# Kernel optimization log

Measured on AMD Instinct MI355X. Metric: run time of the kernel, lower is better.

Reference implementation:

```python
import jax, jax.numpy as jnp
import numpy as np

DN = ('NCHW', 'OIHW', 'NCHW')  # conv dimension numbers
EPS = 1e-5


def _tcn(x, w1, b1, w2, b2, w3, b3):
    """Gated TCN. x: [B,T,N,C] -> [B,T-2,N,Cout].  out = conv1(x)*sigmoid(conv2(x)) + tanh(conv3(x))"""
    xc = jnp.transpose(x, (0, 3, 2, 1))  # [B,C,N,T]
    conv = lambda w, b: jax.lax.conv_general_dilated(xc, w, (1, 1), 'VALID', dimension_numbers=DN) + b[None, :, None, None]
    p = conv(w1, b1)
    q = jax.nn.sigmoid(conv(w2, b2))
    r = jnp.tanh(conv(w3, b3))
    out = p * q + r  # [B,Cout,N,T-2]
    return jnp.transpose(out, (0, 3, 2, 1))


def setup_inputs() -> dict:
    key = jax.random.key(0)
    ks = jax.random.split(key, 16)
    B, T, N, C_in = 32, 24, 1024, 1
    K, C_t, C_s = 3, 64, 16
    inp = {}
    inp['x'] = jax.random.normal(ks[0], (B, T, N, C_in), jnp.float32)
    # stacked Chebyshev polynomials T_0..T_{K-1}, scaled so matmul output stays O(1)
    inp['cheb'] = jax.random.normal(ks[1], (K, N, N), jnp.float32) * (N ** -0.5)
    # temporal conv 1 (C_in -> C_t), kernel (1,3)
    s1 = (2.0 / (C_in * 3 + C_t * 3)) ** 0.5
    for i, nm in enumerate(['t1_w1', 't1_w2', 't1_w3']):
        inp[nm] = jax.random.normal(ks[2 + i], (C_t, C_in, 1, 3), jnp.float32) * s1
        inp[nm.replace('w', 'b')] = jnp.zeros((C_t,), jnp.float32)
    # Chebyshev weights (K, C_t, C_s), xavier-normal
    sc = (2.0 / (C_t + C_s)) ** 0.5
    inp['w_cheb'] = jax.random.normal(ks[5], (K, C_t, C_s), jnp.float32) * sc
    inp['b_cheb'] = jnp.zeros((C_s,), jnp.float32)
    # temporal conv 2 (C_s -> C_s)
    s2 = (2.0 / (C_s * 3 + C_s * 3)) ** 0.5
    for i, nm in enumerate(['t2_w1', 't2_w2', 't2_w3']):
        inp[nm] = jax.random.normal(ks[6 + i], (C_s, C_s, 1, 3), jnp.float32) * s2
        inp[nm.replace('w', 'b')] = jnp.zeros((C_s,), jnp.float32)
    # BatchNorm2d over num_nodes channel
    inp['bn_gamma'] = jnp.ones((N,), jnp.float32)
    inp['bn_beta'] = jnp.zeros((N,), jnp.float32)
    return inp


def reference(x, cheb, t1_w1, t1_b1, t1_w2, t1_b2, t1_w3, t1_b3,
              w_cheb, b_cheb, t2_w1, t2_b1, t2_w2, t2_b2, t2_w3, t2_b3,
              bn_gamma, bn_beta):
    # gated TCN 1: [B,24,N,1] -> [B,22,N,64]
    h = _tcn(x, t1_w1, t1_b1, t1_w2, t1_b2, t1_w3, t1_b3)
    # Chebyshev graph conv fused over all time steps and K taps:
    # T_k_x[b,t,n,c] = sum_m h[b,t,m,c] * cheb[k,m,n]; out = sum_k T_k_x @ W[k]
    s = jnp.einsum('btmc,kmn,kco->btno', h, cheb, w_cheb) + b_cheb  # [B,22,N,16]
    # gated TCN 2: -> [B,20,N,16]
    h2 = _tcn(s, t2_w1, t2_b1, t2_w2, t2_b2, t2_w3, t2_b3)
    # BatchNorm2d over node dim (training-mode batch stats), matching permute(0,2,1,3)
    y = jnp.transpose(h2, (0, 2, 1, 3))  # [B,N,T',C]
    mean = jnp.mean(y, axis=(0, 2, 3), keepdims=True)
    var = jnp.var(y, axis=(0, 2, 3), keepdims=True)  # biased, like torch BN
    y = (y - mean) * jax.lax.rsqrt(var + EPS) * bn_gamma[None, :, None, None] + bn_beta[None, :, None, None]
    y = jnp.transpose(y, (0, 2, 1, 3))  # [B,T',N,C]
    return jax.nn.relu(y)
```

## Files before the change

### kernel.cpp

```cpp
#include <hip/hip_runtime.h>
#include <hip/hip_bf16.h>

using bf16x8 = __attribute__((ext_vector_type(8))) short;
using bf16x4 = __attribute__((ext_vector_type(4))) short;
using f32x4  = __attribute__((ext_vector_type(4))) float;
using f32x2  = __attribute__((ext_vector_type(2))) float;

static __device__ __forceinline__ float bf2f(short s) {
  union { unsigned u; float f; } z;
  z.u = ((unsigned)(unsigned short)s) << 16;
  return z.f;
}
static __device__ __forceinline__ short f2bfs(float f) {
  union { __hip_bfloat16 h; short s; } u;
  u.h = __float2bfloat16(f);
  return u.s;
}
static __device__ __forceinline__ float frcp(float x) { return __builtin_amdgcn_rcpf(x); }
static __device__ __forceinline__ float sigm_f(float x) { return frcp(1.f + __expf(-x)); }
static __device__ __forceinline__ float tanh_f(float x) {
  return fmaf(2.f, frcp(1.f + __expf(-2.f * x)), -1.f);
}

typedef const __attribute__((address_space(1))) unsigned int* gas_u32;
typedef __attribute__((address_space(3))) unsigned int* las_u32;
#define GLOAD16(gp, lp) __builtin_amdgcn_global_load_lds( \
    (gas_u32)(const void*)(gp), (las_u32)(void*)(lp), 16, 0, 0)

__global__ void __launch_bounds__(256) k_front(
    const float* __restrict__ x,
    const float* __restrict__ w1, const float* __restrict__ b1,
    const float* __restrict__ w2, const float* __restrict__ b2,
    const float* __restrict__ w3, const float* __restrict__ b3,
    const float* __restrict__ wcheb,
    __hip_bfloat16* __restrict__ hwt, int bt0, int ch,
    const float* __restrict__ cheb, __hip_bfloat16* __restrict__ chebT) {
  __shared__ __align__(16) char smem[32768];
  const int tid = threadIdx.x;

  if ((int)blockIdx.x >= ch * 4) {
    float (*tile)[65] = reinterpret_cast<float (*)[65]>(smem);
    int blk = blockIdx.x - ch * 4;
    int k = blk >> 8;
    int rem = blk & 255;
    int m0 = (rem >> 4) << 6;
    int n0 = (rem & 15) << 6;
    int tx = tid & 63;
    int ty = tid >> 6;
    const float* src = cheb + (size_t)k * 1024 * 1024;
    #pragma unroll
    for (int i = 0; i < 16; i++) {
      int ml = ty + i * 4;
      tile[ml][tx] = src[(size_t)(m0 + ml) * 1024 + n0 + tx];
    }
    __syncthreads();
    #pragma unroll
    for (int i = 0; i < 16; i++) {
      int nl = ty + i * 4;
      chebT[(size_t)(n0 + nl) * 3072 + k * 1024 + m0 + tx] =
          __float2bfloat16(tile[tx][nl]);
    }
    return;
  }

  char* hls = smem;
  const int lane = tid & 63, w = tid >> 6;
  const int r16 = lane & 15, kb = lane >> 4;
  const int btl = blockIdx.x >> 2;
  const int m0 = (blockIdx.x & 3) << 8;
  const int bt = bt0 + btl;
  const int b = bt / 22, t = bt % 22;

  const float* xp = x + (size_t)(b * 24 + t) * 1024 + m0 + tid;
  const float x0 = xp[0], x1 = xp[1024], x2 = xp[2048];
  const f32x2 x0v = {x0, x0}, x1v = {x1, x1}, x2v = {x2, x2};

  bf16x8 bw[3][2];
  #pragma unroll
  for (int kk = 0; kk < 3; kk++)
    #pragma unroll
    for (int ks = 0; ks < 2; ks++)
      #pragma unroll
      for (int jj = 0; jj < 8; jj++)
        bw[kk][ks][jj] = f2bfs(wcheb[kk * 1024 + (ks * 32 + kb * 8 + jj) * 16 + r16]);

  const int rswz = (tid & 7) << 4;
  #pragma unroll
  for (int cg = 0; cg < 8; cg++) {
    bf16x8 hv;
    #pragma unroll
    for (int j2 = 0; j2 < 4; j2++) {
      const int c2 = cg * 4 + j2;
      const int wi = 6 * c2;
      f32x2 pw = {b1[2*c2], b1[2*c2+1]};
      f32x2 qw = {b2[2*c2], b2[2*c2+1]};
      f32x2 rw = {b3[2*c2], b3[2*c2+1]};
      pw = __builtin_elementwise_fma(x0v, (f32x2){w1[wi], w1[wi+3]}, pw);
      qw = __builtin_elementwise_fma(x0v, (f32x2){w2[wi], w2[wi+3]}, qw);
      rw = __builtin_elementwise_fma(x0v, (f32x2){w3[wi], w3[wi+3]}, rw);
      pw = __builtin_elementwise_fma(x1v, (f32x2){w1[wi+1], w1[wi+4]}, pw);
      qw = __builtin_elementwise_fma(x1v, (f32x2){w2[wi+1], w2[wi+4]}, qw);
      rw = __builtin_elementwise_fma(x1v, (f32x2){w3[wi+1], w3[wi+4]}, rw);
      pw = __builtin_elementwise_fma(x2v, (f32x2){w1[wi+2], w1[wi+5]}, pw);
      qw = __builtin_elementwise_fma(x2v, (f32x2){w2[wi+2], w2[wi+5]}, qw);
      rw = __builtin_elementwise_fma(x2v, (f32x2){w3[wi+2], w3[wi+5]}, rw);
      hv[j2*2+0] = f2bfs(fmaf(pw.x, sigm_f(qw.x), tanh_f(rw.x)));
      hv[j2*2+1] = f2bfs(fmaf(pw.y, sigm_f(qw.y), tanh_f(rw.y)));
    }
    *(bf16x8*)(hls + tid * 128 + ((cg << 4) ^ rswz)) = hv;
  }
  __syncthreads();

  const char* Ab = hls + (w * 64 + r16) * 128;
  const int axor = (r16 & 7) << 4;
  f32x4 acc[4][3];
  #pragma unroll
  for (int mt = 0; mt < 4; mt++)
    #pragma unroll
    for (int kk = 0; kk < 3; kk++) acc[mt][kk] = (f32x4){0.f, 0.f, 0.f, 0.f};

  #pragma unroll
  for (int ks = 0; ks < 2; ks++) {
    #pragma unroll
    for (int mt = 0; mt < 4; mt++) {
      bf16x8 a = *(const bf16x8*)(Ab + mt * 2048 + ((((ks << 2) + kb) << 4) ^ axor));
      #pragma unroll
      for (int kk = 0; kk < 3; kk++)
        acc[mt][kk] = __builtin_amdgcn_mfma_f32_16x16x32_bf16(a, bw[kk][ks], acc[mt][kk], 0, 0, 0);
    }
  }

  __hip_bfloat16* hp = hwt + (size_t)btl * 49152 + r16 * 3072 + m0 + w * 64;
  #pragma unroll
  for (int kk = 0; kk < 3; kk++)
    #pragma unroll
    for (int mt = 0; mt < 4; mt++) {
      bf16x4 v;
      #pragma unroll
      for (int r = 0; r < 4; r++) v[r] = f2bfs(acc[mt][kk][r]);
      *(bf16x4*)(hp + kk * 1024 + mt * 16 + kb * 4) = v;
    }
}

__global__ void __launch_bounds__(256, 2) k_gemm(
    const __hip_bfloat16* __restrict__ chebT,
    const __hip_bfloat16* __restrict__ hwt,
    const float* __restrict__ b_cheb,
    __hip_bfloat16* __restrict__ sbuf,
    int bt_base) {
  __shared__ __align__(16) char smem[32768];
  const int tid = threadIdx.x;
  const int lane = tid & 63;
  const int w = tid >> 6;

  int nt, ct;
  if (gridDim.x == 704) {
    const int xcd = blockIdx.x & 7;
    const int idx = blockIdx.x >> 3;
    nt = ((xcd >> 2) << 2) + (idx & 3);
    ct = (xcd & 3) * 22 + (idx >> 2);
  } else {
    nt = blockIdx.x & 7;
    ct = blockIdx.x >> 3;
  }

  const int srow = tid >> 3;
  const int sswz = ((tid & 7) ^ (srow & 7)) << 4;
  const char* Ag = (const char*)chebT + (size_t)(nt * 128 + srow) * 6144 + sswz;
  const int btl = srow >> 4, so = srow & 15;
  const char* Bg = (const char*)hwt + (size_t)(ct * 8 + btl) * 98304 + (size_t)so * 6144 + sswz;
  char* Als = smem + w * 1024;
  char* Bls = smem + 16384 + w * 1024;

  const int r16 = lane & 15;
  const int c16 = lane >> 4;
  const int wr = (w >> 1) << 6;
  const int wc = (w & 1) << 6;
  const int axor = (r16 & 7) << 4;
  const char* Abase = smem + (wr + r16) * 128;
  const char* Bbase = smem + 16384 + (wc + r16) * 128;

  f32x4 acc[4][4];
  #pragma unroll
  for (int i = 0; i < 4; i++)
    #pragma unroll
    for (int j = 0; j < 4; j++) acc[i][j] = (f32x4){0.f, 0.f, 0.f, 0.f};

  for (int kt = 0; kt < 48; kt++) {
    __syncthreads();
    const char* a = Ag + kt * 128;
    const char* b = Bg + kt * 128;
    #pragma unroll
    for (int i = 0; i < 4; i++) GLOAD16(a + i * 196608, Als + i * 4096);
    #pragma unroll
    for (int i = 0; i < 4; i++) GLOAD16(b + i * 196608, Bls + i * 4096);
    __syncthreads();
    #pragma unroll
    for (int ksub = 0; ksub < 2; ksub++) {
      const int ko = (ksub * 64 + c16 * 16) ^ axor;
      bf16x8 af[4], bfr[4];
      #pragma unroll
      for (int i = 0; i < 4; i++) af[i] = *(const bf16x8*)(Abase + i * 2048 + ko);
      #pragma unroll
      for (int j = 0; j < 4; j++) bfr[j] = *(const bf16x8*)(Bbase + j * 2048 + ko);
      #pragma unroll
      for (int i = 0; i < 4; i++)
        #pragma unroll
        for (int j = 0; j < 4; j++)
          acc[i][j] = __builtin_amdgcn_mfma_f32_16x16x32_bf16(af[i], bfr[j], acc[i][j], 0, 0, 0);
    }
  }

  float bias = b_cheb[r16];
  #pragma unroll
  for (int j = 0; j < 4; j++) {
    int gcol = ct * 128 + wc + j * 16 + r16;
    size_t bt_g = (size_t)bt_base + (gcol >> 4);
    int o = gcol & 15;
    #pragma unroll
    for (int i = 0; i < 4; i++) {
      int n0 = nt * 128 + wr + i * 16 + c16 * 4;
      __hip_bfloat16* sp = sbuf + (bt_g * 1024 + n0) * 16 + o;
      #pragma unroll
      for (int r = 0; r < 4; r++)
        sp[r * 16] = __float2bfloat16(acc[i][j][r] + bias);
    }
  }
}

__global__ void __launch_bounds__(256) k_tcn2(
    const __hip_bfloat16* __restrict__ sbuf,
    const float* __restrict__ w1, const float* __restrict__ b1,
    const float* __restrict__ w2, const float* __restrict__ b2,
    const float* __restrict__ w3, const float* __restrict__ b3,
    __hip_bfloat16* __restrict__ h2b) {
  const int tid = threadIdx.x;
  const int lane = tid & 63, w = tid >> 6;
  const int r16 = lane & 15, kb = lane >> 4;
  const int half = blockIdx.x & 1;
  const int bt2 = blockIdx.x >> 1;
  const int b = bt2 / 20, t2 = bt2 % 20;

  bf16x8 bw[3][2];
  const float* wps[3] = {w1, w2, w3};
  #pragma unroll
  for (int c = 0; c < 3; c++) {
    #pragma unroll
    for (int jj = 0; jj < 8; jj++) {
      int k = kb * 8 + jj;
      bw[c][0][jj] = f2bfs(wps[c][r16 * 48 + (k & 15) * 3 + (k >> 4)]);
      bw[c][1][jj] = (kb < 2) ? f2bfs(wps[c][r16 * 48 + (kb * 8 + jj) * 3 + 2]) : (short)0;
    }
  }
  const float bp = b1[r16], bq = b2[r16], br = b3[r16];

  const char* sb = (const char*)sbuf;
  const size_t slice = (size_t)1024 * 32;
  const int rowbase = half * 512 + w * 128;
  const char* baseA = sb + (size_t)(b * 22 + t2 + (kb >> 1)) * slice
                      + (size_t)(rowbase + r16) * 32 + (kb & 1) * 16;
  const char* baseC = sb + (size_t)(b * 22 + t2 + 2) * slice
                      + (size_t)(rowbase + r16) * 32 + (kb & 1) * 16;
  __hip_bfloat16* outp = h2b + ((size_t)bt2 * 1024 + rowbase + kb * 4) * 16 + r16;

  const f32x4 zro = {0.f, 0.f, 0.f, 0.f};
  #pragma unroll 2
  for (int i = 0; i < 8; i++) {
    bf16x8 a0 = *(const bf16x8*)(baseA + i * 512);
    bf16x8 a1{};
    if (kb < 2) a1 = *(const bf16x8*)(baseC + i * 512);
    f32x4 ap = __builtin_amdgcn_mfma_f32_16x16x32_bf16(a0, bw[0][0], zro, 0, 0, 0);
    f32x4 aq = __builtin_amdgcn_mfma_f32_16x16x32_bf16(a0, bw[1][0], zro, 0, 0, 0);
    f32x4 ar = __builtin_amdgcn_mfma_f32_16x16x32_bf16(a0, bw[2][0], zro, 0, 0, 0);
    ap = __builtin_amdgcn_mfma_f32_16x16x32_bf16(a1, bw[0][1], ap, 0, 0, 0);
    aq = __builtin_amdgcn_mfma_f32_16x16x32_bf16(a1, bw[1][1], aq, 0, 0, 0);
    ar = __builtin_amdgcn_mfma_f32_16x16x32_bf16(a1, bw[2][1], ar, 0, 0, 0);
    #pragma unroll
    for (int r = 0; r < 4; r++) {
      float h = fmaf(ap[r] + bp, sigm_f(aq[r] + bq), tanh_f(ar[r] + br));
      outp[(size_t)(i * 16 + r) * 16] = __float2bfloat16(h);
    }
  }
}

__global__ void __launch_bounds__(256) k_bnstats(
    const __hip_bfloat16* __restrict__ h2b, const float* __restrict__ gamma,
    const float* __restrict__ beta, float* __restrict__ out) {
  __shared__ __align__(16) short col[10240];
  __shared__ float rs[4], rs2[4];
  const int n = blockIdx.x;
  const int tid = threadIdx.x;
  const int part = tid & 1;
  float s = 0.f, s2 = 0.f;
  for (int bt2 = tid >> 1; bt2 < 640; bt2 += 128) {
    bf16x8 v = *(const bf16x8*)((const char*)h2b +
        ((size_t)bt2 * 1024 + n) * 32 + part * 16);
    *(bf16x8*)((char*)col + bt2 * 32 + part * 16) = v;
    #pragma unroll
    for (int j = 0; j < 8; j++) { float f = bf2f(v[j]); s += f; s2 += f * f; }
  }
  #pragma unroll
  for (int off = 32; off; off >>= 1) { s += __shfl_down(s, off); s2 += __shfl_down(s2, off); }
  if ((tid & 63) == 0) { rs[tid >> 6] = s; rs2[tid >> 6] = s2; }
  __syncthreads();
  const float S  = rs[0] + rs[1] + rs[2] + rs[3];
  const float S2 = rs2[0] + rs2[1] + rs2[2] + rs2[3];
  const float mean = S * (1.f / 10240.f);
  const float var  = S2 * (1.f / 10240.f) - mean * mean;
  const float a = gamma[n] * rsqrtf(var + 1e-5f);
  const float c = beta[n] - mean * a;

  for (int bt2 = tid >> 1; bt2 < 640; bt2 += 128) {
    bf16x8 v = *(const bf16x8*)((const char*)col + bt2 * 32 + part * 16);
    float4* op = reinterpret_cast<float4*>(out + ((size_t)bt2 * 1024 + n) * 16 + part * 8);
    float4 o0, o1;
    o0.x = fmaxf(0.f, fmaf(bf2f(v[0]), a, c));
    o0.y = fmaxf(0.f, fmaf(bf2f(v[1]), a, c));
    o0.z = fmaxf(0.f, fmaf(bf2f(v[2]), a, c));
    o0.w = fmaxf(0.f, fmaf(bf2f(v[3]), a, c));
    o1.x = fmaxf(0.f, fmaf(bf2f(v[4]), a, c));
    o1.y = fmaxf(0.f, fmaf(bf2f(v[5]), a, c));
    o1.z = fmaxf(0.f, fmaf(bf2f(v[6]), a, c));
    o1.w = fmaxf(0.f, fmaf(bf2f(v[7]), a, c));
    op[0] = o0;
    op[1] = o1;
  }
}

extern "C" void kernel_launch(void* const* d_in, const int* in_sizes, int n_in,
                              void* d_out, int out_size, void* d_ws, size_t ws_size,
                              hipStream_t stream) {
  const float* x     = (const float*)d_in[0];
  const float* cheb  = (const float*)d_in[1];
  const float* t1w1  = (const float*)d_in[2];
  const float* t1b1  = (const float*)d_in[3];
  const float* t1w2  = (const float*)d_in[4];
  const float* t1b2  = (const float*)d_in[5];
  const float* t1w3  = (const float*)d_in[6];
  const float* t1b3  = (const float*)d_in[7];
  const float* wch   = (const float*)d_in[8];
  const float* bch   = (const float*)d_in[9];
  const float* t2w1  = (const float*)d_in[10];
  const float* t2b1  = (const float*)d_in[11];
  const float* t2w2  = (const float*)d_in[12];
  const float* t2b2  = (const float*)d_in[13];
  const float* t2w3  = (const float*)d_in[14];
  const float* t2b3  = (const float*)d_in[15];
  const float* gam   = (const float*)d_in[16];
  const float* bet   = (const float*)d_in[17];

  char* ws = (char*)d_ws;
  __hip_bfloat16* chebT = (__hip_bfloat16*)ws;
  __hip_bfloat16* sbuf  = (__hip_bfloat16*)(ws + 6291456);
  __hip_bfloat16* h2b   = (__hip_bfloat16*)(ws + 29360128);
  __hip_bfloat16* hwt   = (__hip_bfloat16*)(ws + 50331648);

  size_t avail = ws_size > 50331648 ? ws_size - 50331648 : 0;
  int maxch = (int)(avail / 98304);
  maxch &= ~7;
  if (maxch > 704) maxch = 704;
  if (maxch < 8) maxch = 8;

  int first = 1;
  for (int bt0 = 0; bt0 < 704; bt0 += maxch) {
    int ch = (704 - bt0 < maxch) ? (704 - bt0) : maxch;
    int extra = first ? 768 : 0;
    k_front<<<ch * 4 + extra, 256, 0, stream>>>(
        x, t1w1, t1b1, t1w2, t1b2, t1w3, t1b3, wch, hwt, bt0, ch, cheb, chebT);
    k_gemm<<<ch, 256, 0, stream>>>(chebT, hwt, bch, sbuf, bt0);
    first = 0;
  }

  k_tcn2<<<1280, 256, 0, stream>>>(sbuf, t2w1, t2b1, t2w2, t2b2, t2w3, t2b3, h2b);
  k_bnstats<<<1024, 256, 0, stream>>>(h2b, gam, bet, (float*)d_out);
}
```

Measured before the change: 168.0 us.

## Fuse BatchNorm statistics into TCN2 epilogue via atomics, add elementwise BN-ReLU kernel

Per-node sum and sum-of-squares are now computed inside the second gated-TCN kernel with 16-lane shuffle reductions and global float atomicAdds into a zeroed workspace buffer. The separate per-node stats kernel, which re-read h2b with strided accesses and staged it in LDS, is replaced by a fully coalesced elementwise normalize-plus-ReLU kernel. This drops one full strided pass over h2b but adds many atomics (two per node per row group) and a memset, and makes the float accumulation order nondeterministic.

```diff
diff --git a/kernel.cpp b/kernel.cpp
--- a/kernel.cpp
+++ b/kernel.cpp
@@ -233,7 +233,7 @@
     const float* __restrict__ w1, const float* __restrict__ b1,
     const float* __restrict__ w2, const float* __restrict__ b2,
     const float* __restrict__ w3, const float* __restrict__ b3,
-    __hip_bfloat16* __restrict__ h2b) {
+    __hip_bfloat16* __restrict__ h2b, float* __restrict__ sums) {
   const int tid = threadIdx.x;
   const int lane = tid & 63, w = tid >> 6;
   const int r16 = lane & 15, kb = lane >> 4;
@@ -279,52 +279,45 @@
     for (int r = 0; r < 4; r++) {
       float h = fmaf(ap[r] + bp, sigm_f(aq[r] + bq), tanh_f(ar[r] + br));
       outp[(size_t)(i * 16 + r) * 16] = __float2bfloat16(h);
-    }
-  }
-}
-
-__global__ void __launch_bounds__(256) k_bnstats(
-    const __hip_bfloat16* __restrict__ h2b, const float* __restrict__ gamma,
-    const float* __restrict__ beta, float* __restrict__ out) {
-  __shared__ __align__(16) short col[10240];
-  __shared__ float rs[4], rs2[4];
-  const int n = blockIdx.x;
-  const int tid = threadIdx.x;
-  const int part = tid & 1;
-  float s = 0.f, s2 = 0.f;
-  for (int bt2 = tid >> 1; bt2 < 640; bt2 += 128) {
-    bf16x8 v = *(const bf16x8*)((const char*)h2b +
-        ((size_t)bt2 * 1024 + n) * 32 + part * 16);
-    *(bf16x8*)((char*)col + bt2 * 32 + part * 16) = v;
-    #pragma unroll
-    for (int j = 0; j < 8; j++) { float f = bf2f(v[j]); s += f; s2 += f * f; }
-  }
-  #pragma unroll
-  for (int off = 32; off; off >>= 1) { s += __shfl_down(s, off); s2 += __shfl_down(s2, off); }
-  if ((tid & 63) == 0) { rs[tid >> 6] = s; rs2[tid >> 6] = s2; }
-  __syncthreads();
-  const float S  = rs[0] + rs[1] + rs[2] + rs[3];
-  const float S2 = rs2[0] + rs2[1] + rs2[2] + rs2[3];
-  const float mean = S * (1.f / 10240.f);
-  const float var  = S2 * (1.f / 10240.f) - mean * mean;
-  const float a = gamma[n] * rsqrtf(var + 1e-5f);
-  const float c = beta[n] - mean * a;
-
-  for (int bt2 = tid >> 1; bt2 < 640; bt2 += 128) {
-    bf16x8 v = *(const bf16x8*)((const char*)col + bt2 * 32 + part * 16);
-    float4* op = reinterpret_cast<float4*>(out + ((size_t)bt2 * 1024 + n) * 16 + part * 8);
-    float4 o0, o1;
-    o0.x = fmaxf(0.f, fmaf(bf2f(v[0]), a, c));
-    o0.y = fmaxf(0.f, fmaf(bf2f(v[1]), a, c));
-    o0.z = fmaxf(0.f, fmaf(bf2f(v[2]), a, c));
-    o0.w = fmaxf(0.f, fmaf(bf2f(v[3]), a, c));
-    o1.x = fmaxf(0.f, fmaf(bf2f(v[4]), a, c));
-    o1.y = fmaxf(0.f, fmaf(bf2f(v[5]), a, c));
-    o1.z = fmaxf(0.f, fmaf(bf2f(v[6]), a, c));
-    o1.w = fmaxf(0.f, fmaf(bf2f(v[7]), a, c));
-    op[0] = o0;
-    op[1] = o1;
-  }
+      float hs = h, hs2 = h * h;
+      #pragma unroll
+      for (int m = 1; m < 16; m <<= 1) {
+        hs  += __shfl_xor(hs, m, 16);
+        hs2 += __shfl_xor(hs2, m, 16);
+      }
+      if (r16 == 0) {
+        int n = rowbase + kb * 4 + i * 16 + r;
+        atomicAdd(&sums[n], hs);
+        atomicAdd(&sums[1024 + n], hs2);
+      }
+    }
+  }
+}
+
+__global__ void __launch_bounds__(256) k_bnrelu(
+    const __hip_bfloat16* __restrict__ h2b, const float* __restrict__ sums,
+    const float* __restrict__ gamma, const float* __restrict__ beta,
+    float* __restrict__ out) {
+  size_t c = (size_t)blockIdx.x * 256 + threadIdx.x;
+  int n = (int)((c >> 1) & 1023);
+  float S = sums[n], S2 = sums[1024 + n];
+  float mean = S * (1.f / 10240.f);
+  float var  = S2 * (1.f / 10240.f) - mean * mean;
+  float a  = gamma[n] * rsqrtf(var + 1e-5f);
+  float cc = beta[n] - mean * a;
+  bf16x8 v = *(const bf16x8*)((const char*)h2b + c * 16);
+  float4* op = reinterpret_cast<float4*>(out + c * 8);
+  float4 o0, o1;
+  o0.x = fmaxf(0.f, fmaf(bf2f(v[0]), a, cc));
+  o0.y = fmaxf(0.f, fmaf(bf2f(v[1]), a, cc));
+  o0.z = fmaxf(0.f, fmaf(bf2f(v[2]), a, cc));
+  o0.w = fmaxf(0.f, fmaf(bf2f(v[3]), a, cc));
+  o1.x = fmaxf(0.f, fmaf(bf2f(v[4]), a, cc));
+  o1.y = fmaxf(0.f, fmaf(bf2f(v[5]), a, cc));
+  o1.z = fmaxf(0.f, fmaf(bf2f(v[6]), a, cc));
+  o1.w = fmaxf(0.f, fmaf(bf2f(v[7]), a, cc));
+  op[0] = o0;
+  op[1] = o1;
 }
 
 extern "C" void kernel_launch(void* const* d_in, const int* in_sizes, int n_in,
@@ -353,13 +346,16 @@
   __hip_bfloat16* chebT = (__hip_bfloat16*)ws;
   __hip_bfloat16* sbuf  = (__hip_bfloat16*)(ws + 6291456);
   __hip_bfloat16* h2b   = (__hip_bfloat16*)(ws + 29360128);
-  __hip_bfloat16* hwt   = (__hip_bfloat16*)(ws + 50331648);
-
-  size_t avail = ws_size > 50331648 ? ws_size - 50331648 : 0;
+  float*          sums  = (float*)(ws + 50331648);
+  __hip_bfloat16* hwt   = (__hip_bfloat16*)(ws + 50339840);
+
+  size_t avail = ws_size > 50339840 ? ws_size - 50339840 : 0;
   int maxch = (int)(avail / 98304);
   maxch &= ~7;
   if (maxch > 704) maxch = 704;
   if (maxch < 8) maxch = 8;
+
+  hipMemsetAsync(sums, 0, 8192, stream);
 
   int first = 1;
   for (int bt0 = 0; bt0 < 704; bt0 += maxch) {
@@ -371,6 +367,7 @@
     first = 0;
   }
 
-  k_tcn2<<<1280, 256, 0, stream>>>(sbuf, t2w1, t2b1, t2w2, t2b2, t2w3, t2b3, h2b);
-  k_bnstats<<<1024, 256, 0, stream>>>(h2b, gam, bet, (float*)d_out);
-}
+  k_tcn2<<<1280, 256, 0, stream>>>(sbuf, t2w1, t2b1, t2w2, t2b2, t2w3, t2b3,
+                                   h2b, sums);
+  k_bnrelu<<<5120, 256, 0, stream>>>(h2b, sums, gam, bet, (float*)d_out);
+}
```

After: 289.2 us. 1.72x slower.
